# Performance work log

Measured on AMD Instinct MI355X. Metric: run time of the kernel, lower is better.

The kernel has to match this reference:

```python
import jax, jax.numpy as jnp
import numpy as np

HIDDEN = 768
HEADS = 12
ORDERS = 3
NEG = -1e9


def setup_inputs() -> dict:
    key = jax.random.key(0)
    ks = jax.random.split(key, 16)
    B, N = 8, 512
    s = 0.02
    inp = {
        "v": jax.random.normal(ks[0], (B, N, HIDDEN), jnp.float32),
        "k": jax.random.normal(ks[1], (B, N, HIDDEN), jnp.float32),
        "q": jax.random.normal(ks[2], (B, N, HIDDEN), jnp.float32),
        "masks": jax.random.bernoulli(ks[3], 0.1, (ORDERS, B, 1, N, N)),
        "tau": 1,
        "training": 0,
        "Wv": jax.random.normal(ks[4], (HIDDEN, HIDDEN), jnp.float32) * s,
        "bv": jnp.zeros((HIDDEN,), jnp.float32),
        "Wk": jax.random.normal(ks[5], (HIDDEN, HIDDEN), jnp.float32) * s,
        "bk": jnp.zeros((HIDDEN,), jnp.float32),
        "Wq": jax.random.normal(ks[6], (HIDDEN, HIDDEN), jnp.float32) * s,
        "bq": jnp.zeros((HIDDEN,), jnp.float32),
        "Wm": jax.random.normal(ks[7], (HIDDEN, HIDDEN), jnp.float32) * s,
        "bm": jnp.zeros((HIDDEN,), jnp.float32),
        "pool_w": jax.random.normal(ks[8], (HIDDEN, 1), jnp.float32) * s,
        "pool_b": jnp.zeros((1,), jnp.float32),
        "mlp_w1": jax.random.normal(ks[9], (HIDDEN, HIDDEN // 2), jnp.float32) * s,
        "mlp_w2": jax.random.normal(ks[10], (HIDDEN // 2, ORDERS), jnp.float32) * s,
        "mlp_b2": jnp.zeros((ORDERS,), jnp.float32),
    }
    return inp


def _soft_routing(x, pool_w, pool_b, mlp_w1, mlp_w2, mlp_b2):
    # pooling='fc': masked attention pooling over sequence, then 2-layer MLP + softmax
    pad = (jnp.sum(jnp.abs(x), axis=-1) == 0)[:, :, None]        # [B, N, 1]
    scores = x @ pool_w + pool_b                                  # [B, N, 1]
    scores = jnp.where(pad, NEG, scores)
    scores = jax.nn.softmax(scores, axis=1)
    pooled = jnp.sum(x * scores, axis=1)                          # [B, HIDDEN]
    logits = jax.nn.relu(pooled @ mlp_w1) @ mlp_w2 + mlp_b2       # [B, L]
    return jax.nn.softmax(logits, axis=-1)


def reference(v, k, q, masks, tau, training, Wv, bv, Wk, bk, Wq, bq, Wm, bm,
              pool_w, pool_b, mlp_w1, mlp_w2, mlp_b2):
    B, N, _ = q.shape
    dk = HIDDEN // HEADS
    alphas = _soft_routing(v, pool_w, pool_b, mlp_w1, mlp_w2, mlp_b2)  # [B, L]

    def split_heads(x):
        return x.reshape(B, N, HEADS, dk).transpose(0, 2, 1, 3)  # [B, H, N, dk]

    vh = split_heads(v @ Wv + bv)
    kh = split_heads(k @ Wk + bk)
    qh = split_heads(q @ Wq + bq)

    scores = jnp.einsum('bhnd,bhmd->bhnm', qh, kh) / jnp.sqrt(jnp.float32(dk))
    # masks: [L, B, 1, N, N] broadcast over heads -> att_list [L, B, H, N, N]
    masked = jnp.where(masks[:, :, :, :, :], NEG, scores[None])
    att_list = jax.nn.softmax(masked, axis=-1)                    # [L, B, H, N, N]
    att_map = jnp.einsum('bl,lbhnm->bhnm', alphas, att_list)
    atted = jnp.einsum('bhnm,bhmd->bhnd', att_map, vh)
    atted = atted.transpose(0, 2, 1, 3).reshape(B, N, HIDDEN)
    return atted @ Wm + bm
```

## Files before the change

### kernel.cpp

```cpp
#include <hip/hip_runtime.h>
#include <hip/hip_bf16.h>
#include <stdint.h>


typedef __bf16 bf16x8 __attribute__((ext_vector_type(8)));
typedef float f32x4 __attribute__((ext_vector_type(4)));

#define NEGV -1e9f
#define SBFE(x, off) (((int)((x) << (31 - (off)))) >> 31)

__device__ __forceinline__ float b2f(unsigned short h) {
    union { unsigned int u; float f; } x; x.u = ((unsigned int)h) << 16; return x.f;
}
__device__ __forceinline__ unsigned short f2b(float f) {
    union { float f; unsigned int u; } x; x.f = f;
    unsigned int u = x.u + 0x7FFFu + ((x.u >> 16) & 1u);
    return (unsigned short)(u >> 16);
}
__device__ __forceinline__ unsigned int packbf(unsigned int u0, unsigned int u1) {
    unsigned int r0 = (u0 + 0x7FFFu + ((u0 >> 16) & 1u)) >> 16;
    unsigned int r1 = (u1 + 0x7FFFu + ((u1 >> 16) & 1u)) & 0xFFFF0000u;
    return r0 | r1;
}
__device__ __forceinline__ uint4 load8bf(const void* base, size_t elemOff, int isF32) {
    if (!isF32) return *(const uint4*)((const unsigned short*)base + elemOff);
    const uint4* f = (const uint4*)((const float*)base + elemOff);
    uint4 a = f[0], b = f[1];
    uint4 r;
    r.x = packbf(a.x, a.y);
    r.y = packbf(a.z, a.w);
    r.z = packbf(b.x, b.y);
    r.w = packbf(b.z, b.w);
    return r;
}
__device__ __forceinline__ float loadF(const void* p, int idx, int isF32) {
    return isF32 ? ((const float*)p)[idx] : b2f(((const unsigned short*)p)[idx]);
}

__global__ void sniff_kernel(const unsigned int* __restrict__ mp,
                             const unsigned int* __restrict__ vp,
                             const unsigned int* __restrict__ wp,
                             int* __restrict__ flags)
{
    __shared__ int oki, oku, okf, badv, badw;
    if (threadIdx.x == 0) { oki = 1; oku = 1; okf = 1; badv = 0; badw = 0; }
    __syncthreads();
    int li = 1, lu = 1, lf = 1, bv = 0, bw = 0;
    const uint4* m4 = (const uint4*)mp;
    for (int i = threadIdx.x; i < 4096; i += 256) {
        uint4 u = m4[i];
        unsigned int ws[4] = {u.x, u.y, u.z, u.w};
        #pragma unroll
        for (int j = 0; j < 4; j++) {
            unsigned int w = ws[j];
            if (w > 1u) li = 0;
            if (w & 0xFEFEFEFEu) lu = 0;
            if (w != 0u && w != 0x3F800000u) lf = 0;
        }
    }
    const uint4* v4 = (const uint4*)vp;
    const uint4* w4 = (const uint4*)wp;
    for (int i = threadIdx.x; i < 2048; i += 256) {
        uint4 u = v4[i];
        uint4 u2 = w4[i];
        unsigned int wa[4] = {u.x, u.y, u.z, u.w};
        unsigned int wb[4] = {u2.x, u2.y, u2.z, u2.w};
        #pragma unroll
        for (int j = 0; j < 4; j++) {
            float f0 = b2f((unsigned short)(wa[j] & 0xFFFF));
            float f1 = b2f((unsigned short)(wa[j] >> 16));
            if (!(fabsf(f0) < 1e4f) || !(fabsf(f1) < 1e4f)) bv = 1;
            f0 = b2f((unsigned short)(wb[j] & 0xFFFF));
            f1 = b2f((unsigned short)(wb[j] >> 16));
            if (!(fabsf(f0) < 1e4f) || !(fabsf(f1) < 1e4f)) bw = 1;
        }
    }
    if (!li) atomicAnd(&oki, 0);
    if (!lu) atomicAnd(&oku, 0);
    if (!lf) atomicAnd(&okf, 0);
    if (bv) atomicOr(&badv, 1);
    if (bw) atomicOr(&badw, 1);
    __syncthreads();
    if (threadIdx.x == 0) {
        flags[0] = oki ? 0 : (oku ? 1 : (okf ? 2 : 3));
        flags[1] = badv;
        flags[2] = badw;
    }
}

__global__ __launch_bounds__(256) void conv_act_kernel(
        const void* __restrict__ v, const void* __restrict__ k,
        const void* __restrict__ q, const int* __restrict__ flags,
        unsigned short* __restrict__ vb, unsigned short* __restrict__ kb,
        unsigned short* __restrict__ qb)
{
    const int dtV = flags[1];
    const int which = blockIdx.y;
    const void* src = (which == 0) ? v : (which == 1) ? k : q;
    unsigned short* dst = (which == 0) ? vb : (which == 1) ? kb : qb;
    size_t off = ((size_t)blockIdx.x * 256 + threadIdx.x) * 8;
    uint4 r = load8bf(src, off, dtV);
    *(uint4*)(dst + off) = r;
}

__global__ __launch_bounds__(256) void conv_wt_kernel(
        const void* __restrict__ W0, const void* __restrict__ W1,
        const void* __restrict__ W2, const void* __restrict__ W3,
        const int* __restrict__ flags,
        unsigned short* __restrict__ T0, unsigned short* __restrict__ T1,
        unsigned short* __restrict__ T2, unsigned short* __restrict__ T3)
{
    __shared__ unsigned short tile[64][65];
    const int t = threadIdx.x;
    const int dtW = flags[2];
    const int which = blockIdx.y;
    const void* W = (which == 0) ? W0 : (which == 1) ? W1 : (which == 2) ? W2 : W3;
    unsigned short* T = (which == 0) ? T0 : (which == 1) ? T1 : (which == 2) ? T2 : T3;
    const int tk = (blockIdx.x / 12) << 6;
    const int tn = (blockIdx.x % 12) << 6;
    #pragma unroll
    for (int i = 0; i < 16; i++) {
        int idx = (i << 8) + t;
        int r = idx >> 6, c = idx & 63;
        tile[r][c] = f2b(loadF(W, (tk + r) * 768 + tn + c, dtW));
    }
    __syncthreads();
    #pragma unroll
    for (int i = 0; i < 16; i++) {
        int idx = (i << 8) + t;
        int rn = idx >> 6, ck = idx & 63;
        T[(size_t)(tn + rn) * 768 + tk + ck] = tile[ck][rn];
    }
}

__global__ __launch_bounds__(256) void pack_kernel(
        const void* __restrict__ masks, const int* __restrict__ flags,
        unsigned int* __restrict__ pm)
{
    __shared__ unsigned char flg[32 * 512];
    const int t = threadIdx.x;
    const int mode = flags[0];
    const size_t e0 = (size_t)blockIdx.x * (32 * 512);
    if (mode == 0 || mode == 2) {
        const uint4* p = (const uint4*)((const unsigned int*)masks + e0);
        for (int i = t; i < 4096; i += 256) {
            uint4 u = p[i];
            int base = i << 2;
            flg[base + 0] = u.x ? 1 : 0;
            flg[base + 1] = u.y ? 1 : 0;
            flg[base + 2] = u.z ? 1 : 0;
            flg[base + 3] = u.w ? 1 : 0;
        }
    } else if (mode == 1) {
        const uint4* p = (const uint4*)((const unsigned char*)masks + e0);
        for (int i = t; i < 1024; i += 256) {
            uint4 u = p[i];
            unsigned int uu[4] = {u.x, u.y, u.z, u.w};
            int base = i << 4;
            #pragma unroll
            for (int k2 = 0; k2 < 4; k2++)
                #pragma unroll
                for (int bb = 0; bb < 4; bb++)
                    flg[base + k2 * 4 + bb] = ((uu[k2] >> (bb * 8)) & 0xFFu) ? 1 : 0;
        }
    } else {
        const uint4* p = (const uint4*)((const unsigned short*)masks + e0);
        for (int i = t; i < 2048; i += 256) {
            uint4 u = p[i];
            unsigned int uu[4] = {u.x, u.y, u.z, u.w};
            int base = i << 3;
            #pragma unroll
            for (int k2 = 0; k2 < 4; k2++) {
                flg[base + k2 * 2 + 0] = (uu[k2] & 0xFFFFu) ? 1 : 0;
                flg[base + k2 * 2 + 1] = (uu[k2] >> 16) ? 1 : 0;
            }
        }
    }
    __syncthreads();
    const int lbi = blockIdx.x >> 4;
    const int qb0 = (blockIdx.x & 15) << 1;
    for (int widx = t; widx < 512; widx += 256) {
        const int qq = widx >> 8, sub = widx & 255;
        const int w2 = sub >> 6, lm = (sub >> 2) & 15, quad = sub & 3;
        const unsigned char* fr = &flg[(((qq << 4) + (quad << 2)) << 9) + lm];
        unsigned int bits = 0;
        #pragma unroll
        for (int rg = 0; rg < 4; rg++)
            #pragma unroll
            for (int nt = 0; nt < 8; nt++)
                bits |= ((unsigned int)(fr[(rg << 9) + (((w2 << 3) + nt) << 4)] & 1u))
                        << ((rg << 3) + nt);
        pm[(size_t)lbi * 8192 + (size_t)(qb0 + qq) * 256 + sub] = bits;
    }
}

__global__ __launch_bounds__(256) void route_score_kernel(
        const void* __restrict__ v, const void* __restrict__ pool_w,
        const void* __restrict__ pool_b, const int* __restrict__ flags,
        float* __restrict__ scores)
{
    __shared__ float pw[768];
    const int t = threadIdx.x;
    const int b = blockIdx.x >> 3, ch = blockIdx.x & 7;
    const int dtV = flags[1], dtW = flags[2];
    for (int d = t; d < 768; d += 256) pw[d] = loadF(pool_w, d, dtW);
    __syncthreads();
    const int r = t >> 2, c4 = t & 3;
    const int n = (ch << 6) + r;
    float dot = 0.f, asum = 0.f;
    if (!dtV) {
        const unsigned int* vr = (const unsigned int*)v + ((size_t)(b * 512 + n)) * 384;
        for (int j = 0; j < 96; j++) {
            int p = c4 + (j << 2);
            unsigned int u = vr[p];
            float f0 = b2f((unsigned short)(u & 0xFFFF));
            float f1 = b2f((unsigned short)(u >> 16));
            asum += fabsf(f0) + fabsf(f1);
            dot += f0 * pw[2 * p] + f1 * pw[2 * p + 1];
        }
    } else {
        const float* vf = (const float*)v + ((size_t)(b * 512 + n)) * 768;
        for (int j = 0; j < 48; j++) {
            float4 u = ((const float4*)vf)[c4 + (j << 2)];
            int e = (c4 + (j << 2)) << 2;
            asum += fabsf(u.x) + fabsf(u.y) + fabsf(u.z) + fabsf(u.w);
            dot += u.x * pw[e] + u.y * pw[e + 1] + u.z * pw[e + 2] + u.w * pw[e + 3];
        }
    }
    dot += __shfl_xor(dot, 1); dot += __shfl_xor(dot, 2);
    asum += __shfl_xor(asum, 1); asum += __shfl_xor(asum, 2);
    if (c4 == 0)
        scores[b * 512 + n] = (asum == 0.f) ? NEGV : dot + loadF(pool_b, 0, dtW);
}

__global__ __launch_bounds__(512) void route_softmax_kernel(
        const float* __restrict__ scores, float* __restrict__ scs)
{
    __shared__ float red[8];
    const int t = threadIdx.x, b = blockIdx.x;
    float scv = scores[b * 512 + t];
    float mx = scv;
    #pragma unroll
    for (int off = 1; off < 64; off <<= 1) mx = fmaxf(mx, __shfl_xor(mx, off));
    if ((t & 63) == 0) red[t >> 6] = mx;
    __syncthreads();
    float M = red[0];
    #pragma unroll
    for (int i = 1; i < 8; i++) M = fmaxf(M, red[i]);
    float e = __expf(scv - M);
    __syncthreads();
    float sm = e;
    #pragma unroll
    for (int off = 1; off < 64; off <<= 1) sm += __shfl_xor(sm, off);
    if ((t & 63) == 0) red[t >> 6] = sm;
    __syncthreads();
    float SS = 0.f;
    #pragma unroll
    for (int i = 0; i < 8; i++) SS += red[i];
    scs[b * 512 + t] = e / SS;
}

__global__ __launch_bounds__(256) void route_pool_kernel(
        const void* __restrict__ v, const int* __restrict__ flags,
        const float* __restrict__ scs, float* __restrict__ ppart)
{
    __shared__ float ps[64];
    const int t = threadIdx.x;
    const int ch = blockIdx.x, b = blockIdx.y;
    const int dtV = flags[1];
    if (t < 64) ps[t] = scs[b * 512 + (ch << 6) + t];
    __syncthreads();
    const int d0 = t * 3;
    float a0 = 0.f, a1 = 0.f, a2 = 0.f;
    if (!dtV) {
        const unsigned short* vb = (const unsigned short*)v
            + ((size_t)(b * 512 + (ch << 6))) * 768 + d0;
        #pragma unroll 4
        for (int r = 0; r < 64; r++) {
            float p = ps[r];
            a0 += b2f(vb[0]) * p; a1 += b2f(vb[1]) * p; a2 += b2f(vb[2]) * p;
            vb += 768;
        }
    } else {
        const float* vb = (const float*)v + ((size_t)(b * 512 + (ch << 6))) * 768 + d0;
        #pragma unroll 4
        for (int r = 0; r < 64; r++) {
            float p = ps[r];
            a0 += vb[0] * p; a1 += vb[1] * p; a2 += vb[2] * p;
            vb += 768;
        }
    }
    float* o = ppart + ((size_t)(b * 8 + ch)) * 768 + d0;
    o[0] = a0; o[1] = a1; o[2] = a2;
}

__global__ __launch_bounds__(256) void route_hid_kernel(
        const void* __restrict__ w1, const void* __restrict__ w2,
        const int* __restrict__ flags, const float* __restrict__ ppart,
        float* __restrict__ plog)
{
    __shared__ float pool[768];
    __shared__ float red[4][32];
    const int t = threadIdx.x;
    const int jc = blockIdx.x, b = blockIdx.y;
    const int dtW = flags[2];
    for (int d = t; d < 768; d += 256) {
        float a = 0.f;
        #pragma unroll
        for (int c = 0; c < 8; c++) a += ppart[((size_t)(b * 8 + c)) * 768 + d];
        pool[d] = a;
    }
    __syncthreads();
    const int jo = (t & 3) << 3;
    const int dr = t >> 2;
    float acc[8];
    #pragma unroll
    for (int j = 0; j < 8; j++) acc[j] = 0.f;
    for (int it = 0; it < 12; it++) {
        int d = (it << 6) + dr;
        float pv = pool[d];
        size_t off = (size_t)d * 384 + (jc << 5) + jo;
        if (!dtW) {
            uint4 u = *(const uint4*)((const unsigned short*)w1 + off);
            unsigned int uu[4] = {u.x, u.y, u.z, u.w};
            #pragma unroll
            for (int j2 = 0; j2 < 4; j2++) {
                acc[2 * j2]     += pv * b2f((unsigned short)(uu[j2] & 0xFFFF));
                acc[2 * j2 + 1] += pv * b2f((unsigned short)(uu[j2] >> 16));
            }
        } else {
            const float4* f = (const float4*)((const float*)w1 + off);
            float4 u0 = f[0], u1 = f[1];
            acc[0] += pv * u0.x; acc[1] += pv * u0.y;
            acc[2] += pv * u0.z; acc[3] += pv * u0.w;
            acc[4] += pv * u1.x; acc[5] += pv * u1.y;
            acc[6] += pv * u1.z; acc[7] += pv * u1.w;
        }
    }
    #pragma unroll
    for (int off = 4; off < 64; off <<= 1)
        #pragma unroll
        for (int j = 0; j < 8; j++) acc[j] += __shfl_xor(acc[j], off);
    const int w = t >> 6, lane = t & 63;
    if (lane < 4) {
        #pragma unroll
        for (int j = 0; j < 8; j++) red[w][lane * 8 + j] = acc[j];
    }
    __syncthreads();
    if (t < 32) {
        float h = red[0][t] + red[1][t] + red[2][t] + red[3][t];
        h = fmaxf(h, 0.f);
        int jg = (jc << 5) + t;
        float l0 = h * loadF(w2, jg * 3 + 0, dtW);
        float l1 = h * loadF(w2, jg * 3 + 1, dtW);
        float l2 = h * loadF(w2, jg * 3 + 2, dtW);
        #pragma unroll
        for (int off = 1; off < 32; off <<= 1) {
            l0 += __shfl_xor(l0, off);
            l1 += __shfl_xor(l1, off);
            l2 += __shfl_xor(l2, off);
        }
        if (t == 0) {
            float* o = plog + ((size_t)(b * 12 + jc)) * 3;
            o[0] = l0; o[1] = l1; o[2] = l2;
        }
    }
}

__global__ __launch_bounds__(64) void route_alpha_kernel(
        const void* __restrict__ b2, const int* __restrict__ flags,
        const float* __restrict__ plog, float* __restrict__ alphas)
{
    const int t = threadIdx.x, b = blockIdx.x;
    if (t == 0) {
        const int dtW = flags[2];
        float lg[3];
        #pragma unroll
        for (int l = 0; l < 3; l++) {
            float a = loadF(b2, l, dtW);
            for (int jc = 0; jc < 12; jc++) a += plog[((size_t)(b * 12 + jc)) * 3 + l];
            lg[l] = a;
        }
        float mm = fmaxf(lg[0], fmaxf(lg[1], lg[2]));
        float e0 = __expf(lg[0] - mm), e1 = __expf(lg[1] - mm), e2 = __expf(lg[2] - mm);
        float ss = e0 + e1 + e2;
        alphas[b * 3 + 0] = e0 / ss;
        alphas[b * 3 + 1] = e1 / ss;
        alphas[b * 3 + 2] = e2 / ss;
    }
}

__global__ __launch_bounds__(256) void gemm3_kernel(
        const unsigned short* __restrict__ X0, const unsigned short* __restrict__ X1,
        const unsigned short* __restrict__ X2,
        const unsigned short* __restrict__ W0, const unsigned short* __restrict__ W1,
        const unsigned short* __restrict__ W2,
        const void* __restrict__ bias0, const void* __restrict__ bias1,
        const void* __restrict__ bias2,
        const int* __restrict__ flags,
        void* __restrict__ dst0, void* __restrict__ dst1, void* __restrict__ dst2,
        int m0, int m1, int m2)
{
    __shared__ unsigned short smem[8192];
    unsigned short* At = smem;
    unsigned short* Bt = smem + 4096;
    const int t = threadIdx.x;
    const int which = blockIdx.y;
    const unsigned short* X  = (which == 0) ? X0 : (which == 1) ? X1 : X2;
    const unsigned short* WT = (which == 0) ? W0 : (which == 1) ? W1 : W2;
    const void* bias = (which == 0) ? bias0 : (which == 1) ? bias1 : bias2;
    void* dst = (which == 0) ? dst0 : (which == 1) ? dst1 : dst2;
    const int mode = (which == 0) ? m0 : (which == 1) ? m1 : m2;

    const int id = blockIdx.x;
    const int bx = id >> 6, by = id & 63;
    const int row0 = by << 6, col0 = bx << 6;
    const int w = t >> 6, lane = t & 63, quad = lane >> 4, lm = lane & 15;
    const int r0 = t >> 3, c0 = (t & 7) << 3;
    const int wr0 = r0 * 64 + (c0 ^ ((r0 & 7) << 3));
    const int dtW = flags[2];
    const int dtOut = flags[1];

    const unsigned short* xp  = X  + (size_t)(row0 + r0) * 768 + c0;
    const unsigned short* xp2 = xp + 32 * 768;
    const unsigned short* wp  = WT + (size_t)(col0 + r0) * 768 + c0;
    const unsigned short* wp2 = wp + 32 * 768;

    uint4 a0 = *(const uint4*)xp,  a1 = *(const uint4*)xp2;
    uint4 g0 = *(const uint4*)wp,  g1 = *(const uint4*)wp2;

    f32x4 acc[4];
    #pragma unroll
    for (int i = 0; i < 4; i++) acc[i] = (f32x4){0.f, 0.f, 0.f, 0.f};

    const int am = (w << 4) + lm;
    const int abase = am * 64, akey = (am & 7) << 3;

    for (int k0 = 0;;) {
        __syncthreads();
        *(uint4*)&At[wr0] = a0;        *(uint4*)&At[wr0 + 2048] = a1;
        *(uint4*)&Bt[wr0] = g0;        *(uint4*)&Bt[wr0 + 2048] = g1;
        __syncthreads();
        k0 += 64;
        if (k0 < 768) {
            a0 = *(const uint4*)(xp + k0);  a1 = *(const uint4*)(xp2 + k0);
            g0 = *(const uint4*)(wp + k0);  g1 = *(const uint4*)(wp2 + k0);
        }
        #pragma unroll
        for (int ks = 0; ks < 2; ks++) {
            int ko = (quad << 3) + (ks << 5);
            bf16x8 afr = *(const bf16x8*)&At[abase + (ko ^ akey)];
            #pragma unroll
            for (int t4 = 0; t4 < 4; t4++) {
                int bn = (t4 << 4) + lm;
                bf16x8 bfr = *(const bf16x8*)&Bt[bn * 64 + (ko ^ ((bn & 7) << 3))];
                acc[t4] = __builtin_amdgcn_mfma_f32_16x16x32_bf16(afr, bfr, acc[t4], 0, 0, 0);
            }
        }
        if (k0 >= 768) break;
    }

    if (mode == 1 && dtOut) {
        #pragma unroll
        for (int t4 = 0; t4 < 4; t4++) {
            int col = col0 + (t4 << 4) + lm;
            float bsv = loadF(bias, col, dtW);
            #pragma unroll
            for (int rg = 0; rg < 4; rg++) {
                int row = row0 + (w << 4) + (quad << 2) + rg;
                ((float*)dst)[(size_t)row * 768 + col] = acc[t4][rg] + bsv;
            }
        }
        return;
    }

    __syncthreads();
    #pragma unroll
    for (int t4 = 0; t4 < 4; t4++) {
        int colL = (t4 << 4) + lm;
        float bsv = loadF(bias, col0 + colL, dtW);
        #pragma unroll
        for (int rg = 0; rg < 4; rg++) {
            int rowL = (w << 4) + (quad << 2) + rg;
            unsigned short hv = f2b(acc[t4][rg] + bsv);
            if (mode == 2) smem[colL * 72 + rowL] = hv;
            else           smem[rowL * 72 + colL] = hv;
        }
    }
    __syncthreads();
    const int g = t >> 2, cc = (t & 3) << 4;
    uint4 o0 = *(const uint4*)&smem[g * 72 + cc];
    uint4 o1 = *(const uint4*)&smem[g * 72 + cc + 8];
    unsigned short* o;
    if (mode == 0) {
        int b = row0 >> 9, n0b = row0 & 511, h = col0 >> 6;
        o = (unsigned short*)dst + ((size_t)(b * 12 + h) * 512 + n0b + g) * 64 + cc;
    } else if (mode == 2) {
        int b = row0 >> 9, n0b = row0 & 511, h = col0 >> 6;
        o = (unsigned short*)dst + ((size_t)(b * 12 + h) * 64 + g) * 512 + n0b + cc;
    } else {
        o = (unsigned short*)dst + (size_t)(row0 + g) * 768 + col0 + cc;
    }
    *(uint4*)o = o0;
    *(uint4*)(o + 8) = o1;
}

__global__ __launch_bounds__(256) void attn_kernel(
        const unsigned short* __restrict__ qh, const unsigned short* __restrict__ kh,
        const unsigned short* __restrict__ vT, const unsigned int* __restrict__ pm,
        const float* __restrict__ alphas, unsigned short* __restrict__ atted)
{
    __shared__ unsigned short P[16 * 512];
    __shared__ float Zp[4][16][3];
    __shared__ unsigned short Ost[16 * 72];
    const int t = threadIdx.x;
    const int w = t >> 6, lane = t & 63, quad = lane >> 4, lm = lane & 15;
    const int id = blockIdx.x;
    const int bh = id % 96, qb = id / 96;
    const int b = bh / 12, h = bh % 12;
    const int n0 = qb << 4;

    const unsigned int* pmb = pm + (size_t)b * 8192 + (size_t)qb * 256
                                 + (w << 6) + (lm << 2) + quad;
    const unsigned int mw0 = pmb[0];
    const unsigned int mw1 = pmb[65536];
    const unsigned int mw2 = pmb[131072];

    float al[3];
    #pragma unroll
    for (int l = 0; l < 3; l++) al[l] = alphas[b * 3 + l];

    const unsigned short* qrow = qh + ((size_t)(bh * 512 + n0 + lm)) * 64 + (quad << 3);
    bf16x8 qa0 = *(const bf16x8*)qrow;
    bf16x8 qa1 = *(const bf16x8*)(qrow + 32);
    f32x4 acc[8];
    #pragma unroll
    for (int i = 0; i < 8; i++) acc[i] = (f32x4){0.f, 0.f, 0.f, 0.f};
    const unsigned short* kb0 = kh + ((size_t)(bh * 512 + (w << 7) + lm)) * 64 + (quad << 3);
    #pragma unroll
    for (int nt = 0; nt < 8; nt++) {
        const unsigned short* kr = kb0 + nt * (16 * 64);
        bf16x8 k0 = *(const bf16x8*)kr;
        bf16x8 k1 = *(const bf16x8*)(kr + 32);
        acc[nt] = __builtin_amdgcn_mfma_f32_16x16x32_bf16(qa0, k0, acc[nt], 0, 0, 0);
        acc[nt] = __builtin_amdgcn_mfma_f32_16x16x32_bf16(qa1, k1, acc[nt], 0, 0, 0);
    }

    #pragma unroll
    for (int nt = 0; nt < 8; nt++)
        #pragma unroll
        for (int rg = 0; rg < 4; rg++)
            acc[nt][rg] = __expf(acc[nt][rg] * 0.125f);

    const unsigned int im0 = ~mw0, im1 = ~mw1, im2 = ~mw2;

    #pragma unroll
    for (int rg = 0; rg < 4; rg++) {
        float z0 = 0.f, z1 = 0.f, z2 = 0.f;
        #pragma unroll
        for (int nt = 0; nt < 8; nt++) {
            const int bp = (rg << 3) + nt;
            const unsigned int e = __float_as_uint(acc[nt][rg]);
            z0 += __uint_as_float(e & (unsigned int)SBFE(im0, bp));
            z1 += __uint_as_float(e & (unsigned int)SBFE(im1, bp));
            z2 += __uint_as_float(e & (unsigned int)SBFE(im2, bp));
        }
        #pragma unroll
        for (int off = 1; off < 16; off <<= 1) {
            z0 += __shfl_xor(z0, off);
            z1 += __shfl_xor(z1, off);
            z2 += __shfl_xor(z2, off);
        }
        if (lm == 0) {
            int row = (quad << 2) + rg;
            Zp[w][row][0] = z0; Zp[w][row][1] = z1; Zp[w][row][2] = z2;
        }
    }
    __syncthreads();

    #pragma unroll
    for (int rg = 0; rg < 4; rg++) {
        const int row = (quad << 2) + rg;
        float addu = 0.f;
        unsigned int cb[3];
        #pragma unroll
        for (int l = 0; l < 3; l++) {
            float Z = Zp[0][row][l] + Zp[1][row][l] + Zp[2][row][l] + Zp[3][row][l];
            float c;
            if (Z > 0.f) c = al[l] * __builtin_amdgcn_rcpf(Z);
            else { c = 0.f; addu += al[l] * (1.0f / 512.0f); }
            cb[l] = __float_as_uint(c);
        }
        const int key = row & 7;
        const int pbase = row * 512 + (lm & 7) + (w << 7)
                        + ((((lm >> 3) ^ key) & 1) << 3);
        const int kk16 = (key >> 1) << 4;
        #pragma unroll
        for (int nt = 0; nt < 8; nt++) {
            const int bp = (rg << 3) + nt;
            float wsum = __uint_as_float(cb[0] & (unsigned int)SBFE(im0, bp))
                       + __uint_as_float(cb[1] & (unsigned int)SBFE(im1, bp))
                       + __uint_as_float(cb[2] & (unsigned int)SBFE(im2, bp));
            float p = fmaf(acc[nt][rg], wsum, addu);
            unsigned int u = __float_as_uint(p) + 0x8000u;
            P[pbase + ((nt << 4) ^ kk16)] = (unsigned short)(u >> 16);
        }
    }

    const unsigned short* vb = vT + ((size_t)(bh * 64 + (w << 4) + lm)) * 512 + (quad << 3);
    bf16x8 vp0 = *(const bf16x8*)vb;
    bf16x8 vp1 = *(const bf16x8*)(vb + 32);
    __syncthreads();

    f32x4 accO = (f32x4){0.f, 0.f, 0.f, 0.f};
    #pragma unroll
    for (int ks = 0; ks < 16; ks++) {
        bf16x8 pa = *(const bf16x8*)&P[lm * 512 + ((((ks << 2) + quad) ^ (lm & 7)) << 3)];
        bf16x8 vf = (ks == 0) ? vp0 : (ks == 1) ? vp1 : *(const bf16x8*)(vb + (ks << 5));
        accO = __builtin_amdgcn_mfma_f32_16x16x32_bf16(pa, vf, accO, 0, 0, 0);
    }
    #pragma unroll
    for (int rg = 0; rg < 4; rg++) {
        unsigned int u = __float_as_uint(accO[rg]) + 0x8000u;
        Ost[((quad << 2) + rg) * 72 + (w << 4) + lm] = (unsigned short)(u >> 16);
    }
    __syncthreads();
    const int r2 = t >> 4, c4 = t & 15;
    uint2 val = *(const uint2*)&Ost[r2 * 72 + (c4 << 2)];
    *(uint2*)&atted[((size_t)(b * 512 + n0 + r2)) * 768 + (h << 6) + (c4 << 2)] = val;
}

extern "C" void kernel_launch(void* const* d_in, const int* in_sizes, int n_in,
                              void* d_out, int out_size, void* d_ws, size_t ws_size,
                              hipStream_t stream)
{
    const void* v  = d_in[0];
    const void* k  = d_in[1];
    const void* q  = d_in[2];
    const void* mk = d_in[3];
    const void* Wv = d_in[6];
    const void* bv = d_in[7];
    const void* Wk = d_in[8];
    const void* bk = d_in[9];
    const void* Wq = d_in[10];
    const void* bq = d_in[11];
    const void* Wm = d_in[12];
    const void* bm = d_in[13];
    const void* pool_w = d_in[14];
    const void* pool_b = d_in[15];
    const void* w1 = d_in[16];
    const void* w2 = d_in[17];
    const void* b2 = d_in[18];

    char* ws = (char*)d_ws;
    int*   flags  = (int*)ws;
    float* alphas = (float*)(ws + 256);
    float* scores = (float*)(ws + 512);
    float* scs    = (float*)(ws + 16896);
    float* ppart  = (float*)(ws + 33280);
    float* plog   = (float*)(ws + 229888);
    unsigned int* pm = (unsigned int*)(ws + 262144);
    unsigned short* qh  = (unsigned short*)(ws + 1048576);
    unsigned short* kh  = (unsigned short*)(ws + 1048576 + 1 * 6291456L);
    unsigned short* vT  = (unsigned short*)(ws + 1048576 + 2 * 6291456L);
    unsigned short* vb  = (unsigned short*)(ws + 1048576 + 3 * 6291456L);
    unsigned short* kb  = (unsigned short*)(ws + 1048576 + 4 * 6291456L);
    unsigned short* qb  = (unsigned short*)(ws + 1048576 + 5 * 6291456L);
    unsigned short* atted = vb;
    char* wt0 = ws + 1048576 + 6 * 6291456L;
    unsigned short* WTv = (unsigned short*)(wt0);
    unsigned short* WTk = (unsigned short*)(wt0 + 1 * 1179648L);
    unsigned short* WTq = (unsigned short*)(wt0 + 2 * 1179648L);
    unsigned short* WTm = (unsigned short*)(wt0 + 3 * 1179648L);

    sniff_kernel<<<dim3(1), dim3(256), 0, stream>>>(
        (const unsigned int*)mk, (const unsigned int*)v, (const unsigned int*)Wv, flags);
    conv_act_kernel<<<dim3(1536, 3), dim3(256), 0, stream>>>(v, k, q, flags, vb, kb, qb);
    conv_wt_kernel<<<dim3(144, 4), dim3(256), 0, stream>>>(
        Wv, Wk, Wq, Wm, flags, WTv, WTk, WTq, WTm);
    pack_kernel<<<dim3(384), dim3(256), 0, stream>>>(mk, flags, pm);
    route_score_kernel<<<dim3(64), dim3(256), 0, stream>>>(v, pool_w, pool_b, flags, scores);
    route_softmax_kernel<<<dim3(8), dim3(512), 0, stream>>>(scores, scs);
    route_pool_kernel<<<dim3(8, 8), dim3(256), 0, stream>>>(v, flags, scs, ppart);
    route_hid_kernel<<<dim3(12, 8), dim3(256), 0, stream>>>(w1, w2, flags, ppart, plog);
    route_alpha_kernel<<<dim3(8), dim3(64), 0, stream>>>(b2, flags, plog, alphas);
    gemm3_kernel<<<dim3(768, 3), dim3(256), 0, stream>>>(
        vb, kb, qb, WTv, WTk, WTq, bv, bk, bq, flags,
        (void*)vT, (void*)kh, (void*)qh, 2, 0, 0);
    attn_kernel<<<dim3(3072), dim3(256), 0, stream>>>(qh, kh, vT, pm, alphas, atted);
    gemm3_kernel<<<dim3(768, 1), dim3(256), 0, stream>>>(
        atted, atted, atted, WTm, WTm, WTm, bm, bm, bm, flags,
        d_out, d_out, d_out, 1, 1, 1);
}
```

Measured before the change: 276.2 us.

## Process 32 query rows per attention block to reuse K and V loads

Each attention block now handles two 16-row query tiles instead of one, so each K and V fragment loaded from global memory feeds two MFMAs. The grid halves to 1536 blocks and shared memory for P, Zp and Ost doubles. MFMA sections are also wrapped in s_setprio. The trade-off is higher register and LDS use per block, which can lower occupancy, and fewer blocks to spread across the GPU.

After: 273.5 us. Within noise of the previous version (-1.0%).

```diff
diff --git a/kernel.cpp b/kernel.cpp
--- a/kernel.cpp
+++ b/kernel.cpp
@@ -510,100 +510,130 @@
         const unsigned short* __restrict__ vT, const unsigned int* __restrict__ pm,
         const float* __restrict__ alphas, unsigned short* __restrict__ atted)
 {
-    __shared__ unsigned short P[16 * 512];
-    __shared__ float Zp[4][16][3];
-    __shared__ unsigned short Ost[16 * 72];
+    __shared__ unsigned short P[32 * 512];
+    __shared__ float Zp[4][32][3];
+    __shared__ unsigned short Ost[32 * 72];
     const int t = threadIdx.x;
     const int w = t >> 6, lane = t & 63, quad = lane >> 4, lm = lane & 15;
     const int id = blockIdx.x;
-    const int bh = id % 96, qb = id / 96;
+    const int bh = id % 96, qb2 = id / 96;
     const int b = bh / 12, h = bh % 12;
-    const int n0 = qb << 4;
-
-    const unsigned int* pmb = pm + (size_t)b * 8192 + (size_t)qb * 256
+    const int n0 = qb2 << 5;
+
+    const unsigned int* pmb = pm + (size_t)b * 8192 + (size_t)(qb2 << 1) * 256
                                  + (w << 6) + (lm << 2) + quad;
-    const unsigned int mw0 = pmb[0];
-    const unsigned int mw1 = pmb[65536];
-    const unsigned int mw2 = pmb[131072];
+    unsigned int mw[2][3];
+    #pragma unroll
+    for (int s = 0; s < 2; s++) {
+        mw[s][0] = pmb[s * 256];
+        mw[s][1] = pmb[s * 256 + 65536];
+        mw[s][2] = pmb[s * 256 + 131072];
+    }
 
     float al[3];
     #pragma unroll
     for (int l = 0; l < 3; l++) al[l] = alphas[b * 3 + l];
 
-    const unsigned short* qrow = qh + ((size_t)(bh * 512 + n0 + lm)) * 64 + (quad << 3);
-    bf16x8 qa0 = *(const bf16x8*)qrow;
-    bf16x8 qa1 = *(const bf16x8*)(qrow + 32);
-    f32x4 acc[8];
-    #pragma unroll
-    for (int i = 0; i < 8; i++) acc[i] = (f32x4){0.f, 0.f, 0.f, 0.f};
+    bf16x8 qa[2][2];
+    #pragma unroll
+    for (int s = 0; s < 2; s++) {
+        const unsigned short* qrow = qh + ((size_t)(bh * 512 + n0 + (s << 4) + lm)) * 64
+                                        + (quad << 3);
+        qa[s][0] = *(const bf16x8*)qrow;
+        qa[s][1] = *(const bf16x8*)(qrow + 32);
+    }
+
+    f32x4 acc[2][8];
+    #pragma unroll
+    for (int s = 0; s < 2; s++)
+        #pragma unroll
+        for (int i = 0; i < 8; i++) acc[s][i] = (f32x4){0.f, 0.f, 0.f, 0.f};
+
     const unsigned short* kb0 = kh + ((size_t)(bh * 512 + (w << 7) + lm)) * 64 + (quad << 3);
+    __builtin_amdgcn_s_setprio(1);
     #pragma unroll
     for (int nt = 0; nt < 8; nt++) {
         const unsigned short* kr = kb0 + nt * (16 * 64);
         bf16x8 k0 = *(const bf16x8*)kr;
         bf16x8 k1 = *(const bf16x8*)(kr + 32);
-        acc[nt] = __builtin_amdgcn_mfma_f32_16x16x32_bf16(qa0, k0, acc[nt], 0, 0, 0);
-        acc[nt] = __builtin_amdgcn_mfma_f32_16x16x32_bf16(qa1, k1, acc[nt], 0, 0, 0);
-    }
-
-    #pragma unroll
-    for (int nt = 0; nt < 8; nt++)
-        #pragma unroll
-        for (int rg = 0; rg < 4; rg++)
-            acc[nt][rg] = __expf(acc[nt][rg] * 0.125f);
-
-    const unsigned int im0 = ~mw0, im1 = ~mw1, im2 = ~mw2;
-
-    #pragma unroll
-    for (int rg = 0; rg < 4; rg++) {
-        float z0 = 0.f, z1 = 0.f, z2 = 0.f;
-        #pragma unroll
-        for (int nt = 0; nt < 8; nt++) {
-            const int bp = (rg << 3) + nt;
-            const unsigned int e = __float_as_uint(acc[nt][rg]);
-            z0 += __uint_as_float(e & (unsigned int)SBFE(im0, bp));
-            z1 += __uint_as_float(e & (unsigned int)SBFE(im1, bp));
-            z2 += __uint_as_float(e & (unsigned int)SBFE(im2, bp));
-        }
-        #pragma unroll
-        for (int off = 1; off < 16; off <<= 1) {
-            z0 += __shfl_xor(z0, off);
-            z1 += __shfl_xor(z1, off);
-            z2 += __shfl_xor(z2, off);
-        }
-        if (lm == 0) {
-            int row = (quad << 2) + rg;
-            Zp[w][row][0] = z0; Zp[w][row][1] = z1; Zp[w][row][2] = z2;
-        }
-    }
-    __syncthreads();
-
-    #pragma unroll
-    for (int rg = 0; rg < 4; rg++) {
-        const int row = (quad << 2) + rg;
-        float addu = 0.f;
-        unsigned int cb[3];
-        #pragma unroll
-        for (int l = 0; l < 3; l++) {
-            float Z = Zp[0][row][l] + Zp[1][row][l] + Zp[2][row][l] + Zp[3][row][l];
-            float c;
-            if (Z > 0.f) c = al[l] * __builtin_amdgcn_rcpf(Z);
-            else { c = 0.f; addu += al[l] * (1.0f / 512.0f); }
-            cb[l] = __float_as_uint(c);
-        }
-        const int key = row & 7;
-        const int pbase = row * 512 + (lm & 7) + (w << 7)
-                        + ((((lm >> 3) ^ key) & 1) << 3);
-        const int kk16 = (key >> 1) << 4;
-        #pragma unroll
-        for (int nt = 0; nt < 8; nt++) {
-            const int bp = (rg << 3) + nt;
-            float wsum = __uint_as_float(cb[0] & (unsigned int)SBFE(im0, bp))
-                       + __uint_as_float(cb[1] & (unsigned int)SBFE(im1, bp))
-                       + __uint_as_float(cb[2] & (unsigned int)SBFE(im2, bp));
-            float p = fmaf(acc[nt][rg], wsum, addu);
-            unsigned int u = __float_as_uint(p) + 0x8000u;
-            P[pbase + ((nt << 4) ^ kk16)] = (unsigned short)(u >> 16);
+        acc[0][nt] = __builtin_amdgcn_mfma_f32_16x16x32_bf16(qa[0][0], k0, acc[0][nt], 0, 0, 0);
+        acc[1][nt] = __builtin_amdgcn_mfma_f32_16x16x32_bf16(qa[1][0], k0, acc[1][nt], 0, 0, 0);
+        acc[0][nt] = __builtin_amdgcn_mfma_f32_16x16x32_bf16(qa[0][1], k1, acc[0][nt], 0, 0, 0);
+        acc[1][nt] = __builtin_amdgcn_mfma_f32_16x16x32_bf16(qa[1][1], k1, acc[1][nt], 0, 0, 0);
+    }
+    __builtin_amdgcn_s_setprio(0);
+
+    #pragma unroll
+    for (int s = 0; s < 2; s++)
+        #pragma unroll
+        for (int nt = 0; nt < 8; nt++)
+            #pragma unroll
+            for (int rg = 0; rg < 4; rg++)
+                acc[s][nt][rg] = __expf(acc[s][nt][rg] * 0.125f);
+
+    unsigned int im[2][3];
+    #pragma unroll
+    for (int s = 0; s < 2; s++)
+        #pragma unroll
+        for (int l = 0; l < 3; l++) im[s][l] = ~mw[s][l];
+
+    #pragma unroll
+    for (int s = 0; s < 2; s++) {
+        #pragma unroll
+        for (int rg = 0; rg < 4; rg++) {
+            float z0 = 0.f, z1 = 0.f, z2 = 0.f;
+            #pragma unroll
+            for (int nt = 0; nt < 8; nt++) {
+                const int bp = (rg << 3) + nt;
+                const unsigned int e = __float_as_uint(acc[s][nt][rg]);
+                z0 += __uint_as_float(e & (unsigned int)SBFE(im[s][0], bp));
+                z1 += __uint_as_float(e & (unsigned int)SBFE(im[s][1], bp));
+                z2 += __uint_as_float(e & (unsigned int)SBFE(im[s][2], bp));
+            }
+            #pragma unroll
+            for (int off = 1; off < 16; off <<= 1) {
+                z0 += __shfl_xor(z0, off);
+                z1 += __shfl_xor(z1, off);
+                z2 += __shfl_xor(z2, off);
+            }
+            if (lm == 0) {
+                int row = (s << 4) + (quad << 2) + rg;
+                Zp[w][row][0] = z0; Zp[w][row][1] = z1; Zp[w][row][2] = z2;
+            }
+        }
+    }
+    __syncthreads();
+
+    #pragma unroll
+    for (int s = 0; s < 2; s++) {
+        #pragma unroll
+        for (int rg = 0; rg < 4; rg++) {
+            const int row = (quad << 2) + rg;
+            const int prow = (s << 4) + row;
+            float addu = 0.f;
+            unsigned int cb[3];
+            #pragma unroll
+            for (int l = 0; l < 3; l++) {
+                float Z = Zp[0][prow][l] + Zp[1][prow][l] + Zp[2][prow][l] + Zp[3][prow][l];
+                float c;
+                if (Z > 0.f) c = al[l] * __builtin_amdgcn_rcpf(Z);
+                else { c = 0.f; addu += al[l] * (1.0f / 512.0f); }
+                cb[l] = __float_as_uint(c);
+            }
+            const int key = row & 7;
+            const int pbase = prow * 512 + (lm & 7) + (w << 7)
+                            + ((((lm >> 3) ^ key) & 1) << 3);
+            const int kk16 = (key >> 1) << 4;
+            #pragma unroll
+            for (int nt = 0; nt < 8; nt++) {
+                const int bp = (rg << 3) + nt;
+                float wsum = __uint_as_float(cb[0] & (unsigned int)SBFE(im[s][0], bp))
+                           + __uint_as_float(cb[1] & (unsigned int)SBFE(im[s][1], bp))
+                           + __uint_as_float(cb[2] & (unsigned int)SBFE(im[s][2], bp));
+                float p = fmaf(acc[s][nt][rg], wsum, addu);
+                unsigned int u = __float_as_uint(p) + 0x8000u;
+                P[pbase + ((nt << 4) ^ kk16)] = (unsigned short)(u >> 16);
+            }
         }
     }
 
@@ -612,22 +642,34 @@
     bf16x8 vp1 = *(const bf16x8*)(vb + 32);
     __syncthreads();
 
-    f32x4 accO = (f32x4){0.f, 0.f, 0.f, 0.f};
+    f32x4 accO0 = (f32x4){0.f, 0.f, 0.f, 0.f};
+    f32x4 accO1 = (f32x4){0.f, 0.f, 0.f, 0.f};
+    __builtin_amdgcn_s_setprio(1);
     #pragma unroll
     for (int ks = 0; ks < 16; ks++) {
-        bf16x8 pa = *(const bf16x8*)&P[lm * 512 + ((((ks << 2) + quad) ^ (lm & 7)) << 3)];
+        const int po = ((((ks << 2) + quad) ^ (lm & 7)) << 3);
+        bf16x8 pa0 = *(const bf16x8*)&P[lm * 512 + po];
+        bf16x8 pa1 = *(const bf16x8*)&P[(lm + 16) * 512 + po];
         bf16x8 vf = (ks == 0) ? vp0 : (ks == 1) ? vp1 : *(const bf16x8*)(vb + (ks << 5));
-        accO = __builtin_amdgcn_mfma_f32_16x16x32_bf16(pa, vf, accO, 0, 0, 0);
-    }
+        accO0 = __builtin_amdgcn_mfma_f32_16x16x32_bf16(pa0, vf, accO0, 0, 0, 0);
+        accO1 = __builtin_amdgcn_mfma_f32_16x16x32_bf16(pa1, vf, accO1, 0, 0, 0);
+    }
+    __builtin_amdgcn_s_setprio(0);
     #pragma unroll
     for (int rg = 0; rg < 4; rg++) {
-        unsigned int u = __float_as_uint(accO[rg]) + 0x8000u;
-        Ost[((quad << 2) + rg) * 72 + (w << 4) + lm] = (unsigned short)(u >> 16);
+        unsigned int u0 = __float_as_uint(accO0[rg]) + 0x8000u;
+        unsigned int u1 = __float_as_uint(accO1[rg]) + 0x8000u;
+        Ost[((quad << 2) + rg) * 72 + (w << 4) + lm] = (unsigned short)(u0 >> 16);
+        Ost[(16 + (quad << 2) + rg) * 72 + (w << 4) + lm] = (unsigned short)(u1 >> 16);
     }
     __syncthreads();
     const int r2 = t >> 4, c4 = t & 15;
-    uint2 val = *(const uint2*)&Ost[r2 * 72 + (c4 << 2)];
-    *(uint2*)&atted[((size_t)(b * 512 + n0 + r2)) * 768 + (h << 6) + (c4 << 2)] = val;
+    #pragma unroll
+    for (int rr = 0; rr < 2; rr++) {
+        const int row = (rr << 4) + r2;
+        uint2 val = *(const uint2*)&Ost[row * 72 + (c4 << 2)];
+        *(uint2*)&atted[((size_t)(b * 512 + n0 + row)) * 768 + (h << 6) + (c4 << 2)] = val;
+    }
 }
 
 extern "C" void kernel_launch(void* const* d_in, const int* in_sizes, int n_in,
@@ -687,7 +729,7 @@
     gemm3_kernel<<<dim3(768, 3), dim3(256), 0, stream>>>(
         vb, kb, qb, WTv, WTk, WTq, bv, bk, bq, flags,
         (void*)vT, (void*)kh, (void*)qh, 2, 0, 0);
-    attn_kernel<<<dim3(3072), dim3(256), 0, stream>>>(qh, kh, vT, pm, alphas, atted);
+    attn_kernel<<<dim3(1536), dim3(256), 0, stream>>>(qh, kh, vT, pm, alphas, atted);
     gemm3_kernel<<<dim3(768, 1), dim3(256), 0, stream>>>(
         atted, atted, atted, WTm, WTm, WTm, bm, bm, bm, flags,
         d_out, d_out, d_out, 1, 1, 1);
```
